# Performance work log

Hardware: AMD Instinct MI355X
Metric: run time of the kernel (lower is better)

## Reference

```python
import jax, jax.numpy as jnp
import numpy as np
from jax import lax

BLOCK_LEN = 128  # ctx_len 8192 / blocks 64
NEG_INF = -1e9


def setup_inputs() -> dict:
    key = jax.random.key(0)
    ks = jax.random.split(key, 8)
    N, L, Dm = 2, 8192, 4096
    W, H, dh = 1024, 16, 64  # width = d_model*0.25
    s = lambda fan: 1.0 / np.sqrt(fan)
    return {
        "inputs": jax.random.normal(ks[0], (N, L, Dm), jnp.float32),
        "conv_w": jax.random.normal(ks[1], (3, Dm, 3 * W), jnp.float32) * s(3 * Dm),
        "conv_b": jnp.zeros((3 * W,), jnp.float32),
        "wq": jax.random.normal(ks[2], (W, H, dh), jnp.float32) * s(W),
        "bq": jnp.zeros((H, dh), jnp.float32),
        "wk": jax.random.normal(ks[3], (W, H, dh), jnp.float32) * s(W),
        "bk": jnp.zeros((H, dh), jnp.float32),
        "wv": jax.random.normal(ks[4], (W, H, dh), jnp.float32) * s(W),
        "bv": jnp.zeros((H, dh), jnp.float32),
        "wo": jax.random.normal(ks[5], (H, dh, W), jnp.float32) * s(H * dh),
        "bo": jnp.zeros((W,), jnp.float32),
        "proj_w": jax.random.normal(ks[6], (W, Dm), jnp.float32) * s(W),
        "proj_b": jnp.zeros((Dm,), jnp.float32),
    }


def reference(inputs, conv_w, conv_b, wq, bq, wk, bk, wv, bv, wo, bo, proj_w, proj_b):
    N, L, Dm = inputs.shape
    # Conv1D(kernel=3, same padding) producing q,k,v concatenated
    x = lax.conv_general_dilated(
        inputs, conv_w, window_strides=(1,), padding="SAME",
        dimension_numbers=("NWC", "WIO", "NWC")) + conv_b
    q, k, v = jnp.split(x, 3, axis=-1)  # each [N, L, W]
    W_ = q.shape[-1]
    nb = L // BLOCK_LEN
    # row attention: independent causal attention within each block
    q = q.reshape(N * nb, BLOCK_LEN, W_)
    k = k.reshape(N * nb, BLOCK_LEN, W_)
    v = v.reshape(N * nb, BLOCK_LEN, W_)
    dh = wq.shape[-1]
    qh = jnp.einsum("btd,dhe->bthe", q, wq) + bq  # [B, T, H, dh]
    kh = jnp.einsum("btd,dhe->bthe", k, wk) + bk
    vh = jnp.einsum("btd,dhe->bthe", v, wv) + bv
    scale = 1.0 / jnp.sqrt(jnp.asarray(dh, qh.dtype))
    scores = jnp.einsum("bqhe,bkhe->bhqk", qh * scale, kh)
    causal = jnp.tril(jnp.ones((BLOCK_LEN, BLOCK_LEN), bool))
    scores = jnp.where(causal, scores, NEG_INF)
    p = jax.nn.softmax(scores, axis=-1)
    o = jnp.einsum("bhqk,bkhe->bqhe", p, vh)
    o = jnp.einsum("bqhe,hed->bqd", o, wo) + bo  # MHA output projection -> width
    o = o.reshape(N, L, W_)
    return o @ proj_w + proj_b  # final Dense(d_model)
```

## Files before the change

kernel.cpp:

```cpp
#include <hip/hip_runtime.h>
#include <hip/hip_bf16.h>
#include <stdint.h>

typedef __attribute__((ext_vector_type(8))) short short8;
typedef __attribute__((ext_vector_type(4))) float f32x4;

#define AS1 __attribute__((address_space(1)))
#define AS3 __attribute__((address_space(3)))

__device__ __forceinline__ short f2bf(float x) {
    __hip_bfloat16 h = __float2bfloat16(x);
    union { __hip_bfloat16 h; short s; } u; u.h = h; return u.s;
}

__device__ __forceinline__ void gload_lds16(const short* g, short* l) {
    __builtin_amdgcn_global_load_lds((const AS1 void*)g, (AS3 void*)l, 16, 0, 0);
}

#define BAR()        asm volatile("s_barrier" ::: "memory")
#define VMCNT_BAR(N) asm volatile("s_waitcnt vmcnt(" #N ")\n\ts_barrier" ::: "memory")

template<int TAPS, bool F32OUT>
__global__ __launch_bounds__(512, 2) void gemm256(
    const short* __restrict__ A, int lda,
    const short* __restrict__ BT, int ldb, long long tapB,
    void* __restrict__ Cout, int ldc,
    const float* __restrict__ bias, int Ktiles)
{
    __shared__ __align__(16) short As[2 * 2 * 256 * 32];
    __shared__ __align__(16) short Bs[2 * 2 * 256 * 32];
    const int tid = threadIdx.x, lane = tid & 63, wid = tid >> 6;
    const int wm = wid >> 2, wn = wid & 3;
    const int m0 = blockIdx.y * 256, n0 = blockIdx.x * 256;
    const size_t arow0 = (TAPS == 3) ? ((size_t)(m0 >> 13) * 8194 + (size_t)(m0 & 8191))
                                     : (size_t)m0;
    const size_t ldaS = (size_t)lda, ldbS = (size_t)ldb, tapBS = (size_t)tapB;
    const short* Abase0 = A + arow0 * ldaS;
    const short* Bbase0 = BT + (size_t)n0 * ldbS;
    const int c15 = lane & 15, g4 = (lane >> 4) * 4;
    const int swz = ((lane >> 4) ^ ((c15 >> 1) & 3)) * 8;
    const int srow = tid >> 2;
    const int schunk = (((tid & 3) ^ ((tid >> 3) & 3)) * 8);

#define STG_A(u, kh, buf) do { \
    const int tp_ = (TAPS == 3) ? ((u) >> 6) : 0; \
    const int kc_ = (TAPS == 3) ? (((u) & 63) << 6) : ((u) << 6); \
    const short* g_ = Abase0 + (size_t)tp_ * ldaS + kc_ + (kh) * 32 \
                      + (size_t)srow * ldaS + schunk; \
    short* l_ = As + (buf) * 16384 + (kh) * 8192 + wid * 512; \
    gload_lds16(g_, l_); \
    gload_lds16(g_ + 128 * ldaS, l_ + 4096); \
} while (0)

#define STG_B(u, kh, buf) do { \
    const int tp_ = (TAPS == 3) ? ((u) >> 6) : 0; \
    const int kc_ = (TAPS == 3) ? (((u) & 63) << 6) : ((u) << 6); \
    const short* g_ = Bbase0 + (size_t)tp_ * tapBS + kc_ + (kh) * 32 \
                      + (size_t)srow * ldbS + schunk; \
    short* l_ = Bs + (buf) * 16384 + (kh) * 8192 + wid * 512; \
    gload_lds16(g_, l_); \
    gload_lds16(g_ + 128 * ldbS, l_ + 4096); \
} while (0)

#define LDA_(buf, kk, mi) (*(const short8*)(As + (buf) * 16384 + (kk) * 8192 \
                           + (wm * 128 + (mi) * 16 + c15) * 32 + swz))
#define LDB_(buf, kk, nj) (*(const short8*)(Bs + (buf) * 16384 + (kk) * 8192 \
                           + (wn * 64 + (nj) * 16 + c15) * 32 + swz))

#define MFMA4x4(MB) do { \
    __builtin_amdgcn_s_setprio(1); \
    _Pragma("unroll") \
    for (int mi_ = 0; mi_ < 4; ++mi_) \
        _Pragma("unroll") \
        for (int nj_ = 0; nj_ < 4; ++nj_) \
            acc[(MB) + mi_][nj_] = __builtin_amdgcn_mfma_f32_16x16x32_bf16( \
                af[mi_], bf4[nj_], acc[(MB) + mi_][nj_], 0, 0, 0); \
    __builtin_amdgcn_s_setprio(0); \
} while (0)

    f32x4 acc[8][4];
    #pragma unroll
    for (int i = 0; i < 8; ++i)
        #pragma unroll
        for (int j = 0; j < 4; ++j)
            acc[i][j] = (f32x4){0.f, 0.f, 0.f, 0.f};

    STG_A(0, 0, 0); STG_B(0, 0, 0); STG_A(0, 1, 0); STG_B(0, 1, 0);
    VMCNT_BAR(4);

    for (int t = 0; t < Ktiles; ++t) {
        const int c = t & 1, nb = c ^ 1;
        const bool st = (t + 1 < Ktiles);
        const int u = t + 1;
        short8 af[4], bf4[4];

        #pragma unroll
        for (int mi = 0; mi < 4; ++mi) af[mi] = LDA_(c, 0, mi);
        #pragma unroll
        for (int nj = 0; nj < 4; ++nj) bf4[nj] = LDB_(c, 0, nj);
        if (st) STG_A(u, 0, nb);
        BAR();
        MFMA4x4(0);
        BAR();

        #pragma unroll
        for (int mi = 0; mi < 4; ++mi) af[mi] = LDA_(c, 0, 4 + mi);
        if (st) STG_B(u, 0, nb);
        if (st) { VMCNT_BAR(4); } else { VMCNT_BAR(0); }
        MFMA4x4(4);
        BAR();

        #pragma unroll
        for (int mi = 0; mi < 4; ++mi) af[mi] = LDA_(c, 1, mi);
        #pragma unroll
        for (int nj = 0; nj < 4; ++nj) bf4[nj] = LDB_(c, 1, nj);
        if (st) STG_A(u, 1, nb);
        BAR();
        MFMA4x4(0);
        BAR();

        #pragma unroll
        for (int mi = 0; mi < 4; ++mi) af[mi] = LDA_(c, 1, 4 + mi);
        if (st) STG_B(u, 1, nb);
        if (st) { VMCNT_BAR(4); } else { VMCNT_BAR(0); }
        MFMA4x4(4);
        BAR();
    }

    float bv[4];
    #pragma unroll
    for (int nj = 0; nj < 4; ++nj)
        bv[nj] = bias ? bias[n0 + wn * 64 + nj * 16 + c15] : 0.f;
    #pragma unroll
    for (int mi = 0; mi < 8; ++mi) {
        #pragma unroll
        for (int r = 0; r < 4; ++r) {
            const size_t row = (size_t)m0 + wm * 128 + mi * 16 + g4 + r;
            #pragma unroll
            for (int nj = 0; nj < 4; ++nj) {
                const int col = n0 + wn * 64 + nj * 16 + c15;
                const float v = acc[mi][nj][r] + bv[nj];
                if (F32OUT) ((float*)Cout)[row * (size_t)ldc + col] = v;
                else        ((short*)Cout)[row * (size_t)ldc + col] = f2bf(v);
            }
        }
    }
#undef STG_A
#undef STG_B
#undef LDA_
#undef LDB_
#undef MFMA4x4
}

__global__ __launch_bounds__(256) void attn_kernel(
    const short* __restrict__ qh, const short* __restrict__ kh,
    const short* __restrict__ vh, short* __restrict__ obuf)
{
    __shared__ __align__(16) char smem[54272];
    short* qs = (short*)smem;
    short* ks = (short*)smem + 9216;
    short* vt = (short*)(smem + 36864);
    short* ps = (short*)smem;
    short* os = (short*)smem;

    const int tid = threadIdx.x, lane = tid & 63, wid = tid >> 6;
    const int h = blockIdx.x, b = blockIdx.y;
    const size_t base = (size_t)b * 128 * 1024 + (size_t)h * 64;

    for (int i = tid; i < 1024; i += 256) {
        const int row = i >> 3, c8 = i & 7;
        const size_t g = base + (size_t)row * 1024 + c8 * 8;
        *(short8*)(qs + row * 72 + c8 * 8) = *(const short8*)(qh + g);
        *(short8*)(ks + row * 72 + c8 * 8) = *(const short8*)(kh + g);
        short8 vv = *(const short8*)(vh + g);
        #pragma unroll
        for (int j = 0; j < 8; ++j) vt[(c8 * 8 + j) * 136 + row] = vv[j];
    }
    __syncthreads();

    const int c15 = lane & 15, g8 = (lane >> 4) * 8, g4 = (lane >> 4) * 4;
    const int r0 = wid * 32;

    f32x4 sacc[2][8];
    #pragma unroll
    for (int mi = 0; mi < 2; ++mi)
        #pragma unroll
        for (int nj = 0; nj < 8; ++nj)
            sacc[mi][nj] = (f32x4){0.f, 0.f, 0.f, 0.f};
    #pragma unroll
    for (int kk = 0; kk < 2; ++kk) {
        short8 aq[2];
        #pragma unroll
        for (int mi = 0; mi < 2; ++mi)
            aq[mi] = *(const short8*)(qs + (r0 + mi * 16 + c15) * 72 + kk * 32 + g8);
        #pragma unroll
        for (int nj = 0; nj < 8; ++nj) {
            short8 bk8 = *(const short8*)(ks + (nj * 16 + c15) * 72 + kk * 32 + g8);
            #pragma unroll
            for (int mi = 0; mi < 2; ++mi)
                sacc[mi][nj] = __builtin_amdgcn_mfma_f32_16x16x32_bf16(
                    aq[mi], bk8, sacc[mi][nj], 0, 0, 0);
        }
    }
    __syncthreads();

    #pragma unroll
    for (int mi = 0; mi < 2; ++mi) {
        #pragma unroll
        for (int r = 0; r < 4; ++r) {
            const int qrow = r0 + mi * 16 + g4 + r;
            float m = -3.0e38f, pv[8];
            #pragma unroll
            for (int nj = 0; nj < 8; ++nj) {
                float s = sacc[mi][nj][r] * 0.125f;
                if (nj * 16 + c15 > qrow) s = -1.0e9f;
                pv[nj] = s; m = fmaxf(m, s);
            }
            #pragma unroll
            for (int off = 8; off >= 1; off >>= 1) m = fmaxf(m, __shfl_xor(m, off));
            float sum = 0.f;
            #pragma unroll
            for (int nj = 0; nj < 8; ++nj) { float p = __expf(pv[nj] - m); pv[nj] = p; sum += p; }
            #pragma unroll
            for (int off = 8; off >= 1; off >>= 1) sum += __shfl_xor(sum, off);
            const float inv = 1.0f / sum;
            #pragma unroll
            for (int nj = 0; nj < 8; ++nj)
                ps[qrow * 136 + nj * 16 + c15] = f2bf(pv[nj] * inv);
        }
    }
    __syncthreads();

    f32x4 oacc[2][4];
    #pragma unroll
    for (int mi = 0; mi < 2; ++mi)
        #pragma unroll
        for (int nj = 0; nj < 4; ++nj)
            oacc[mi][nj] = (f32x4){0.f, 0.f, 0.f, 0.f};
    #pragma unroll
    for (int kt = 0; kt < 4; ++kt) {
        short8 ap[2];
        #pragma unroll
        for (int mi = 0; mi < 2; ++mi)
            ap[mi] = *(const short8*)(ps + (r0 + mi * 16 + c15) * 136 + kt * 32 + g8);
        #pragma unroll
        for (int nj = 0; nj < 4; ++nj) {
            short8 bv8 = *(const short8*)(vt + (nj * 16 + c15) * 136 + kt * 32 + g8);
            #pragma unroll
            for (int mi = 0; mi < 2; ++mi)
                oacc[mi][nj] = __builtin_amdgcn_mfma_f32_16x16x32_bf16(
                    ap[mi], bv8, oacc[mi][nj], 0, 0, 0);
        }
    }
    __syncthreads();

    #pragma unroll
    for (int mi = 0; mi < 2; ++mi)
        #pragma unroll
        for (int r = 0; r < 4; ++r)
            #pragma unroll
            for (int nj = 0; nj < 4; ++nj)
                os[(r0 + mi * 16 + g4 + r) * 72 + nj * 16 + c15] = f2bf(oacc[mi][nj][r]);
    __syncthreads();

    for (int i = tid; i < 1024; i += 256) {
        const int row = i >> 3, c8 = i & 7;
        *(short8*)(obuf + base + (size_t)row * 1024 + c8 * 8) =
            *(const short8*)(os + row * 72 + c8 * 8);
    }
}

__global__ void pad_convert_inputs(const float* __restrict__ in, short* __restrict__ out)
{
    const int row = blockIdx.x;
    const int n = row / 8194, l = row % 8194;
    short* orow = out + (size_t)row * 4096;
    if (l == 0 || l == 8193) {
        for (int i = threadIdx.x; i < 512; i += 256) {
            uint4 z; z.x = z.y = z.z = z.w = 0u;
            *(uint4*)(orow + i * 8) = z;
        }
    } else {
        const float* irow = in + ((size_t)n * 8192 + (l - 1)) * 4096;
        for (int i = threadIdx.x; i < 512; i += 256) {
            float4 a = *(const float4*)(irow + i * 8);
            float4 b = *(const float4*)(irow + i * 8 + 4);
            short8 v;
            v[0] = f2bf(a.x); v[1] = f2bf(a.y); v[2] = f2bf(a.z); v[3] = f2bf(a.w);
            v[4] = f2bf(b.x); v[5] = f2bf(b.y); v[6] = f2bf(b.z); v[7] = f2bf(b.w);
            *(short8*)(orow + i * 8) = v;
        }
    }
}

__global__ void transpose_convert(const float* __restrict__ in, short* __restrict__ out,
                                  int R, int C)
{
    __shared__ float tile[32][33];
    const int tx = threadIdx.x & 31, ty = threadIdx.x >> 5;
    const int bx = blockIdx.x * 32, by = blockIdx.y * 32;
    #pragma unroll
    for (int i = 0; i < 32; i += 8)
        tile[ty + i][tx] = in[(size_t)(by + ty + i) * C + bx + tx];
    __syncthreads();
    #pragma unroll
    for (int i = 0; i < 32; i += 8)
        out[(size_t)(bx + ty + i) * R + by + tx] = f2bf(tile[tx][ty + i]);
}

__global__ void convert_bf16(const float* __restrict__ in, short* __restrict__ out, int n8)
{
    const int idx = blockIdx.x * 256 + threadIdx.x;
    if (idx < n8) {
        float4 a = *(const float4*)(in + (size_t)idx * 8);
        float4 b = *(const float4*)(in + (size_t)idx * 8 + 4);
        short8 v;
        v[0] = f2bf(a.x); v[1] = f2bf(a.y); v[2] = f2bf(a.z); v[3] = f2bf(a.w);
        v[4] = f2bf(b.x); v[5] = f2bf(b.y); v[6] = f2bf(b.z); v[7] = f2bf(b.w);
        *(short8*)(out + (size_t)idx * 8) = v;
    }
}

__global__ void fuse_bias(const float* __restrict__ bo, const float* __restrict__ projw,
                          const float* __restrict__ projb, float* __restrict__ outb)
{
    const int j = blockIdx.x * 256 + threadIdx.x;
    float s = projb[j];
    for (int w = 0; w < 1024; ++w) s = fmaf(bo[w], projw[(size_t)w * 4096 + j], s);
    outb[j] = s;
}

extern "C" void kernel_launch(void* const* d_in, const int* in_sizes, int n_in,
                              void* d_out, int out_size, void* d_ws, size_t ws_size,
                              hipStream_t stream)
{
    const float* inputs = (const float*)d_in[0];
    const float* conv_w = (const float*)d_in[1];
    const float* conv_b = (const float*)d_in[2];
    const float* wq     = (const float*)d_in[3];
    const float* bq     = (const float*)d_in[4];
    const float* wk     = (const float*)d_in[5];
    const float* bk     = (const float*)d_in[6];
    const float* wv     = (const float*)d_in[7];
    const float* bv     = (const float*)d_in[8];
    const float* wo     = (const float*)d_in[9];
    const float* bo     = (const float*)d_in[10];
    const float* proj_w = (const float*)d_in[11];
    const float* proj_b = (const float*)d_in[12];

    char* ws = (char*)d_ws;
    short* in_pad = (short*)(ws + 0);
    short* w_bf   = (short*)(ws + 134283264);
    short* qkv    = (short*)(ws + 209780736);
    short* wq_t   = (short*)(ws + 310444032);
    short* wk_t   = (short*)(ws + 312541184);
    short* wv_t   = (short*)(ws + 314638336);
    short* wo_bf  = (short*)(ws + 316735488);
    short* proj_t = (short*)(ws + 318832640);
    short* WfT    = (short*)(ws + 327221248);
    float* bfused = (float*)(ws + 335609856);
    short* qh_buf = (short*)(ws + 0);
    short* kh_buf = (short*)(ws + 33554432);
    short* vh_buf = (short*)(ws + 67108864);
    short* o_buf  = (short*)(ws + 134283264);

    dim3 blk(256), blk5(512);

    pad_convert_inputs<<<16388, blk, 0, stream>>>(inputs, in_pad);
    for (int t = 0; t < 3; ++t)
        transpose_convert<<<dim3(96, 128), blk, 0, stream>>>(
            conv_w + (size_t)t * 4096 * 3072, w_bf + (size_t)t * 3072 * 4096, 4096, 3072);
    transpose_convert<<<dim3(32, 32), blk, 0, stream>>>(wq, wq_t, 1024, 1024);
    transpose_convert<<<dim3(32, 32), blk, 0, stream>>>(wk, wk_t, 1024, 1024);
    transpose_convert<<<dim3(32, 32), blk, 0, stream>>>(wv, wv_t, 1024, 1024);
    transpose_convert<<<dim3(128, 32), blk, 0, stream>>>(proj_w, proj_t, 1024, 4096);
    convert_bf16<<<512, blk, 0, stream>>>(wo, wo_bf, 131072);
    fuse_bias<<<16, blk, 0, stream>>>(bo, proj_w, proj_b, bfused);

    gemm256<1, false><<<dim3(4, 16), blk5, 0, stream>>>(
        proj_t, 1024, wo_bf, 1024, 0, WfT, 1024, nullptr, 16);
    gemm256<3, false><<<dim3(12, 64), blk5, 0, stream>>>(
        in_pad, 4096, w_bf, 4096, (long long)3072 * 4096, qkv, 3072, conv_b, 192);
    gemm256<1, false><<<dim3(4, 64), blk5, 0, stream>>>(
        qkv + 0,    3072, wq_t, 1024, 0, qh_buf, 1024, bq, 16);
    gemm256<1, false><<<dim3(4, 64), blk5, 0, stream>>>(
        qkv + 1024, 3072, wk_t, 1024, 0, kh_buf, 1024, bk, 16);
    gemm256<1, false><<<dim3(4, 64), blk5, 0, stream>>>(
        qkv + 2048, 3072, wv_t, 1024, 0, vh_buf, 1024, bv, 16);

    attn_kernel<<<dim3(16, 128), blk, 0, stream>>>(qh_buf, kh_buf, vh_buf, o_buf);

    gemm256<1, true><<<dim3(16, 64), blk5, 0, stream>>>(
        o_buf, 1024, WfT, 1024, 0, d_out, 4096, bfused, 16);
}
```

Before: 1.672 ms.

## Fold Q/K/V head projections into conv weights to drop per-token GEMMs

```diff
diff --git a/kernel.cpp b/kernel.cpp
--- a/kernel.cpp
+++ b/kernel.cpp
@@ -20,7 +20,7 @@
 #define BAR()        asm volatile("s_barrier" ::: "memory")
 #define VMCNT_BAR(N) asm volatile("s_waitcnt vmcnt(" #N ")\n\ts_barrier" ::: "memory")
 
-template<int TAPS, bool F32OUT>
+template<int TAPS, int MODE, bool F32OUT>
 __global__ __launch_bounds__(512, 2) void gemm256(
     const short* __restrict__ A, int lda,
     const short* __restrict__ BT, int ldb, long long tapB,
@@ -36,7 +36,7 @@
                                      : (size_t)m0;
     const size_t ldaS = (size_t)lda, ldbS = (size_t)ldb, tapBS = (size_t)tapB;
     const short* Abase0 = A + arow0 * ldaS;
-    const short* Bbase0 = BT + (size_t)n0 * ldbS;
+    const short* Bbase0 = BT + (size_t)n0 * ldbS + ((MODE == 1) ? (m0 & ~1023) : 0);
     const int c15 = lane & 15, g4 = (lane >> 4) * 4;
     const int swz = ((lane >> 4) ^ ((c15 >> 1) & 3)) * 8;
     const int srow = tid >> 2;
@@ -153,8 +153,7 @@
 }
 
 __global__ __launch_bounds__(256) void attn_kernel(
-    const short* __restrict__ qh, const short* __restrict__ kh,
-    const short* __restrict__ vh, short* __restrict__ obuf)
+    const short* __restrict__ qkvh, short* __restrict__ obuf)
 {
     __shared__ __align__(16) char smem[54272];
     short* qs = (short*)smem;
@@ -165,14 +164,14 @@
 
     const int tid = threadIdx.x, lane = tid & 63, wid = tid >> 6;
     const int h = blockIdx.x, b = blockIdx.y;
-    const size_t base = (size_t)b * 128 * 1024 + (size_t)h * 64;
+    const size_t base = (size_t)b * 128 * 3072 + (size_t)h * 64;
 
     for (int i = tid; i < 1024; i += 256) {
         const int row = i >> 3, c8 = i & 7;
-        const size_t g = base + (size_t)row * 1024 + c8 * 8;
-        *(short8*)(qs + row * 72 + c8 * 8) = *(const short8*)(qh + g);
-        *(short8*)(ks + row * 72 + c8 * 8) = *(const short8*)(kh + g);
-        short8 vv = *(const short8*)(vh + g);
+        const size_t g = base + (size_t)row * 3072 + c8 * 8;
+        *(short8*)(qs + row * 72 + c8 * 8) = *(const short8*)(qkvh + g);
+        *(short8*)(ks + row * 72 + c8 * 8) = *(const short8*)(qkvh + g + 1024);
+        short8 vv = *(const short8*)(qkvh + g + 2048);
         #pragma unroll
         for (int j = 0; j < 8; ++j) vt[(c8 * 8 + j) * 136 + row] = vv[j];
     }
@@ -265,7 +264,8 @@
 
     for (int i = tid; i < 1024; i += 256) {
         const int row = i >> 3, c8 = i & 7;
-        *(short8*)(obuf + base + (size_t)row * 1024 + c8 * 8) =
+        *(short8*)(obuf + (size_t)b * 128 * 1024 + (size_t)h * 64
+                   + (size_t)row * 1024 + c8 * 8) =
             *(const short8*)(os + row * 72 + c8 * 8);
     }
 }
@@ -328,6 +328,22 @@
     float s = projb[j];
     for (int w = 0; w < 1024; ++w) s = fmaf(bo[w], projw[(size_t)w * 4096 + j], s);
     outb[j] = s;
+}
+
+__global__ void fuse_bias_qkv(const float* __restrict__ conv_b,
+                              const float* __restrict__ wq, const float* __restrict__ bq,
+                              const float* __restrict__ wk, const float* __restrict__ bk,
+                              const float* __restrict__ wv, const float* __restrict__ bv,
+                              float* __restrict__ outb)
+{
+    const int o = blockIdx.x * 256 + threadIdx.x;
+    const int p = o >> 10, e = o & 1023;
+    const float* w = (p == 0) ? wq : (p == 1) ? wk : wv;
+    const float* bb = (p == 0) ? bq : (p == 1) ? bk : bv;
+    const float* cb = conv_b + p * 1024;
+    float s = bb[e];
+    for (int d = 0; d < 1024; ++d) s = fmaf(cb[d], w[(size_t)d * 1024 + e], s);
+    outb[o] = s;
 }
 
 extern "C" void kernel_launch(void* const* d_in, const int* in_sizes, int n_in,
@@ -350,46 +366,40 @@
 
     char* ws = (char*)d_ws;
     short* in_pad = (short*)(ws + 0);
-    short* w_bf   = (short*)(ws + 134283264);
-    short* qkv    = (short*)(ws + 209780736);
+    short* cw_bf  = (short*)(ws + 134283264);
+    short* qkvh   = (short*)(ws + 134283264);
+    short* W2T    = (short*)(ws + 234946560);
     short* wq_t   = (short*)(ws + 310444032);
-    short* wk_t   = (short*)(ws + 312541184);
-    short* wv_t   = (short*)(ws + 314638336);
     short* wo_bf  = (short*)(ws + 316735488);
     short* proj_t = (short*)(ws + 318832640);
     short* WfT    = (short*)(ws + 327221248);
     float* bfused = (float*)(ws + 335609856);
-    short* qh_buf = (short*)(ws + 0);
-    short* kh_buf = (short*)(ws + 33554432);
-    short* vh_buf = (short*)(ws + 67108864);
-    short* o_buf  = (short*)(ws + 134283264);
+    float* b2     = (float*)(ws + 335626240);
+    short* o_buf  = (short*)(ws + 0);
 
     dim3 blk(256), blk5(512);
 
     pad_convert_inputs<<<16388, blk, 0, stream>>>(inputs, in_pad);
-    for (int t = 0; t < 3; ++t)
-        transpose_convert<<<dim3(96, 128), blk, 0, stream>>>(
-            conv_w + (size_t)t * 4096 * 3072, w_bf + (size_t)t * 3072 * 4096, 4096, 3072);
+    convert_bf16<<<18432, blk, 0, stream>>>(conv_w, cw_bf, 4718592);
     transpose_convert<<<dim3(32, 32), blk, 0, stream>>>(wq, wq_t, 1024, 1024);
-    transpose_convert<<<dim3(32, 32), blk, 0, stream>>>(wk, wk_t, 1024, 1024);
-    transpose_convert<<<dim3(32, 32), blk, 0, stream>>>(wv, wv_t, 1024, 1024);
+    transpose_convert<<<dim3(32, 32), blk, 0, stream>>>(wk, wq_t + 1048576, 1024, 1024);
+    transpose_convert<<<dim3(32, 32), blk, 0, stream>>>(wv, wq_t + 2097152, 1024, 1024);
     transpose_convert<<<dim3(128, 32), blk, 0, stream>>>(proj_w, proj_t, 1024, 4096);
     convert_bf16<<<512, blk, 0, stream>>>(wo, wo_bf, 131072);
     fuse_bias<<<16, blk, 0, stream>>>(bo, proj_w, proj_b, bfused);
-
-    gemm256<1, false><<<dim3(4, 16), blk5, 0, stream>>>(
+    fuse_bias_qkv<<<12, blk, 0, stream>>>(conv_b, wq, bq, wk, bk, wv, bv, b2);
+
+    gemm256<1, 0, false><<<dim3(4, 16), blk5, 0, stream>>>(
         proj_t, 1024, wo_bf, 1024, 0, WfT, 1024, nullptr, 16);
-    gemm256<3, false><<<dim3(12, 64), blk5, 0, stream>>>(
-        in_pad, 4096, w_bf, 4096, (long long)3072 * 4096, qkv, 3072, conv_b, 192);
-    gemm256<1, false><<<dim3(4, 64), blk5, 0, stream>>>(
-        qkv + 0,    3072, wq_t, 1024, 0, qh_buf, 1024, bq, 16);
-    gemm256<1, false><<<dim3(4, 64), blk5, 0, stream>>>(
-        qkv + 1024, 3072, wk_t, 1024, 0, kh_buf, 1024, bk, 16);
-    gemm256<1, false><<<dim3(4, 64), blk5, 0, stream>>>(
-        qkv + 2048, 3072, wv_t, 1024, 0, vh_buf, 1024, bv, 16);
-
-    attn_kernel<<<dim3(16, 128), blk, 0, stream>>>(qh_buf, kh_buf, vh_buf, o_buf);
-
-    gemm256<1, true><<<dim3(16, 64), blk5, 0, stream>>>(
+    for (int t = 0; t < 3; ++t)
+        gemm256<1, 1, false><<<dim3(16, 12), blk5, 0, stream>>>(
+            wq_t, 1024, cw_bf + (size_t)t * 4096 * 3072, 3072, 0,
+            W2T + (size_t)t * 3072 * 4096, 4096, nullptr, 16);
+    gemm256<3, 0, false><<<dim3(12, 64), blk5, 0, stream>>>(
+        in_pad, 4096, W2T, 4096, (long long)3072 * 4096, qkvh, 3072, b2, 192);
+
+    attn_kernel<<<dim3(16, 128), blk, 0, stream>>>(qkvh, o_buf);
+
+    gemm256<1, 0, true><<<dim3(16, 64), blk5, 0, stream>>>(
         o_buf, 1024, WfT, 1024, 0, d_out, 4096, bfused, 16);
 }
```

Measured after the change: 1.673 ms. About the same (+0.0%).
